# Optimization experiments

Measured on AMD Instinct MI355X. Metric: run time of the kernel, lower is better.

## Reference

```python
import jax, jax.numpy as jnp
import numpy as np

DECAY_EPS = 1e-8  # matches F.cosine_similarity eps
DECAY_RATE = 0.999  # buffer decay_rate


def setup_inputs() -> dict:
    key = jax.random.key(0)
    ks = jax.random.split(key, 6)
    B, M, D = 256, 65536, 1024
    return {
        "query": jax.random.normal(ks[0], (B, D), dtype=jnp.float32),
        "mem_keys": jax.random.normal(ks[1], (M, D), dtype=jnp.float32),
        "mem_values": jax.random.normal(ks[2], (M, D), dtype=jnp.float32),
        "importance": jax.random.uniform(ks[3], (M,), dtype=jnp.float32),
        "access_times": jax.random.randint(ks[4], (M,), 0, 1000, dtype=jnp.int32),
        "access_counts": jax.random.randint(ks[5], (M,), 1, 50, dtype=jnp.int32),
        "current_time": 1000,
        "top_k": 8,
    }


def reference(query, mem_keys, mem_values, importance, access_times, access_counts, current_time, top_k):
    # Batched version of AdaptiveMemoryBuffer.retrieve.
    # query: [B, D]; mem_keys/mem_values: [M, D]; importance/access_*: [M]
    qn = query / jnp.maximum(jnp.linalg.norm(query, axis=-1, keepdims=True), DECAY_EPS)
    kn = mem_keys / jnp.maximum(jnp.linalg.norm(mem_keys, axis=-1, keepdims=True), DECAY_EPS)
    sim = qn @ kn.T  # [B, M] cosine similarity

    dt = (current_time - access_times).astype(jnp.float32)           # time since access
    retention = jnp.power(jnp.float32(DECAY_RATE), dt)               # forgetting curve
    freq_bonus = jnp.log1p(access_counts.astype(jnp.float32))        # log(1 + count)
    scores = sim * (retention * importance * freq_bonus)[None, :]    # [B, M]

    top_scores, top_idx = jax.lax.top_k(scores, top_k)                # [B, k]
    weights = jax.nn.softmax(top_scores, axis=-1)                     # [B, k]
    combined = jnp.einsum('bk,bkd->bd', weights, mem_values[top_idx]) # weighted gather
    confidence = weights.max(axis=-1)                                 # [B]
    return combined, confidence
```

## Files before the change

kernel.cpp:

```cpp
#include <hip/hip_runtime.h>
#include <hip/hip_bf16.h>
#include <math.h>
#include <float.h>

typedef __attribute__((ext_vector_type(8))) short short8;
typedef __attribute__((ext_vector_type(4))) float f32x4;

namespace {

constexpr int B = 256;
constexpr int M = 65536;
constexpr int D = 1024;
constexpr float DECAY_EPS = 1e-8f;
constexpr float DECAY_RATE = 0.999f;

constexpr int BN = 64;
constexpr int BK = 32;
constexpr int KSTEPS = D / BK;

constexpr int CHUNKS = 8;
constexpr int CHUNK = M / CHUNKS;
constexpr int NCAND = CHUNKS * 8;

__device__ inline ushort f2bf(float f) {
  union { __hip_bfloat16 h; ushort u; } v;
  v.h = __float2bfloat16(f);
  return v.u;
}

__global__ void prep_q_kernel(const float* __restrict__ q, ushort* __restrict__ qnf) {
  const int r = blockIdx.x;
  const int t = threadIdx.x;
  float4 v = reinterpret_cast<const float4*>(q + (size_t)r * D)[t];
  float ss = v.x * v.x + v.y * v.y + v.z * v.z + v.w * v.w;
#pragma unroll
  for (int off = 32; off; off >>= 1) ss += __shfl_down(ss, off, 64);
  __shared__ float red[4];
  if ((t & 63) == 0) red[t >> 6] = ss;
  __syncthreads();
  const float inv = 1.0f / fmaxf(sqrtf(red[0] + red[1] + red[2] + red[3]), DECAY_EPS);
  ushort4 o;
  o.x = f2bf(v.x * inv); o.y = f2bf(v.y * inv);
  o.z = f2bf(v.z * inv); o.w = f2bf(v.w * inv);
  const int k0 = t * 4;
  const int kt = k0 >> 5;
  const int lane_slot = (r & 15) + 16 * ((k0 & 31) >> 3);
  const int j0 = k0 & 7;
  *reinterpret_cast<ushort4*>(qnf + (size_t)(kt * 16 + (r >> 4)) * 512 + lane_slot * 8 + j0) = o;
}

__global__ __launch_bounds__(256) void score_gemm_kernel(
    const ushort* __restrict__ qnf, const float* __restrict__ keys,
    const float* __restrict__ importance, const int* __restrict__ atimes,
    const int* __restrict__ acnts, const int* __restrict__ ctime,
    float* __restrict__ scores) {
  __shared__ alignas(16) ushort Bs[2][BN * BK];
  __shared__ float cscale[BN];

  const int t = threadIdx.x;
  const int lane = t & 63;
  const int w = t >> 6;
  const int jb = blockIdx.x * BN;

  const int rw = t >> 2;
  const int cw = t & 3;
  const float* kptr = keys + (size_t)(jb + rw) * D + cw * 8;
  const int woff = rw * BK + ((cw ^ ((rw >> 1) & 3)) * 8);

  f32x4 acc[4][4];
#pragma unroll
  for (int f = 0; f < 4; ++f)
#pragma unroll
    for (int n = 0; n < 4; ++n) acc[f][n] = (f32x4)(0.0f);

  float kn2 = 0.0f;

  {
    float4 v0 = *reinterpret_cast<const float4*>(kptr);
    float4 v1 = *reinterpret_cast<const float4*>(kptr + 4);
    kn2 += v0.x * v0.x + v0.y * v0.y + v0.z * v0.z + v0.w * v0.w;
    kn2 += v1.x * v1.x + v1.y * v1.y + v1.z * v1.z + v1.w * v1.w;
    short8 pk;
    pk[0] = (short)f2bf(v0.x); pk[1] = (short)f2bf(v0.y);
    pk[2] = (short)f2bf(v0.z); pk[3] = (short)f2bf(v0.w);
    pk[4] = (short)f2bf(v1.x); pk[5] = (short)f2bf(v1.y);
    pk[6] = (short)f2bf(v1.z); pk[7] = (short)f2bf(v1.w);
    *reinterpret_cast<short8*>(&Bs[0][woff]) = pk;
  }
  __syncthreads();

  int roff[4];
#pragma unroll
  for (int nf = 0; nf < 4; ++nf) {
    const int row = nf * 16 + (lane & 15);
    roff[nf] = row * BK + (((lane >> 4) ^ ((row >> 1) & 3)) * 8);
  }

  for (int kt = 0; kt < KSTEPS; ++kt) {
    const int cur = kt & 1;
    float4 nv0, nv1;
    if (kt + 1 < KSTEPS) {
      nv0 = *reinterpret_cast<const float4*>(kptr + (kt + 1) * BK);
      nv1 = *reinterpret_cast<const float4*>(kptr + (kt + 1) * BK + 4);
    }
    short8 a[4];
    const short8* ap = reinterpret_cast<const short8*>(qnf) + (size_t)(kt * 16 + w * 4) * 64 + lane;
#pragma unroll
    for (int f = 0; f < 4; ++f) a[f] = ap[f * 64];
    short8 bb[4];
#pragma unroll
    for (int nf = 0; nf < 4; ++nf)
      bb[nf] = *reinterpret_cast<const short8*>(&Bs[cur][roff[nf]]);
#pragma unroll
    for (int f = 0; f < 4; ++f)
#pragma unroll
      for (int nf = 0; nf < 4; ++nf)
        acc[f][nf] = __builtin_amdgcn_mfma_f32_16x16x32_bf16(a[f], bb[nf], acc[f][nf], 0, 0, 0);
    if (kt + 1 < KSTEPS) {
      kn2 += nv0.x * nv0.x + nv0.y * nv0.y + nv0.z * nv0.z + nv0.w * nv0.w;
      kn2 += nv1.x * nv1.x + nv1.y * nv1.y + nv1.z * nv1.z + nv1.w * nv1.w;
      short8 pk;
      pk[0] = (short)f2bf(nv0.x); pk[1] = (short)f2bf(nv0.y);
      pk[2] = (short)f2bf(nv0.z); pk[3] = (short)f2bf(nv0.w);
      pk[4] = (short)f2bf(nv1.x); pk[5] = (short)f2bf(nv1.y);
      pk[6] = (short)f2bf(nv1.z); pk[7] = (short)f2bf(nv1.w);
      *reinterpret_cast<short8*>(&Bs[cur ^ 1][woff]) = pk;
    }
    __syncthreads();
  }

  kn2 += __shfl_xor(kn2, 1, 64);
  kn2 += __shfl_xor(kn2, 2, 64);
  if (cw == 0) {
    const int j = jb + rw;
    const float dt = (float)(ctime[0] - atimes[j]);
    const float mult = powf(DECAY_RATE, dt) * importance[j] * log1pf((float)acnts[j]);
    cscale[rw] = mult / fmaxf(sqrtf(kn2), DECAY_EPS);
  }
  __syncthreads();

#pragma unroll
  for (int f = 0; f < 4; ++f) {
    const int row0 = (w * 4 + f) * 16 + ((lane >> 4) << 2);
#pragma unroll
    for (int nf = 0; nf < 4; ++nf) {
      const int col = nf * 16 + (lane & 15);
      const float cs = cscale[col];
#pragma unroll
      for (int rr = 0; rr < 4; ++rr)
        scores[(size_t)(row0 + rr) * M + jb + col] = acc[f][nf][rr] * cs;
    }
  }
}

__global__ __launch_bounds__(256) void topk_partial_kernel(
    const float* __restrict__ scores, int* __restrict__ cand_i) {
  const int b = blockIdx.y;
  const int c = blockIdx.x;
  const int t = threadIdx.x;
  const int lane = t & 63, w = t >> 6;
  const float4* base4 = reinterpret_cast<const float4*>(scores + (size_t)b * M + (size_t)c * CHUNK);

  float s8[8];
  int i8[8];
#pragma unroll
  for (int i = 0; i < 8; ++i) { s8[i] = -FLT_MAX; i8[i] = 0; }

  auto ins = [&](float x, int j) {
    if (x > s8[0]) {
#pragma unroll
      for (int i = 0; i < 8; ++i) {
        const bool up = (i < 7) && (x > s8[i + 1]);
        const float ks = (x > s8[i]) ? x : s8[i];
        const int ki = (x > s8[i]) ? j : i8[i];
        s8[i] = up ? s8[i + 1] : ks;
        i8[i] = up ? i8[i + 1] : ki;
      }
    }
  };

  const int jbase = c * CHUNK;
  for (int it = 0; it < CHUNK / (256 * 4); ++it) {
    const int slot = it * 256 + t;
    const float4 v = base4[slot];
    const int j0 = jbase + slot * 4;
    ins(v.x, j0 + 0);
    ins(v.y, j0 + 1);
    ins(v.z, j0 + 2);
    ins(v.w, j0 + 3);
  }

  __shared__ float ls[2048];
  __shared__ int li[2048];
#pragma unroll
  for (int i = 0; i < 8; ++i) { ls[t * 8 + i] = s8[i]; li[t * 8 + i] = i8[i]; }
  __syncthreads();

  __shared__ float rs4[4];
  __shared__ int rp4[4];
  for (int r = 0; r < 8; ++r) {
    float ms = -FLT_MAX;
    int mp = 0;
#pragma unroll
    for (int i = 0; i < 8; ++i) {
      const float v = ls[i * 256 + t];
      if (v > ms) { ms = v; mp = i * 256 + t; }
    }
#pragma unroll
    for (int off = 32; off; off >>= 1) {
      const float ov = __shfl_xor(ms, off, 64);
      const int op = __shfl_xor(mp, off, 64);
      if (ov > ms) { ms = ov; mp = op; }
    }
    if (lane == 0) { rs4[w] = ms; rp4[w] = mp; }
    __syncthreads();
    if (t == 0) {
      float bs = -FLT_MAX;
      int bp = 0;
#pragma unroll
      for (int i = 0; i < 4; ++i)
        if (rs4[i] > bs) { bs = rs4[i]; bp = rp4[i]; }
      cand_i[((size_t)b * CHUNKS + c) * 8 + r] = li[bp];
      ls[bp] = -FLT_MAX;
    }
    __syncthreads();
  }
}

__global__ __launch_bounds__(512) void rescore_kernel(
    const int* __restrict__ cand_i, const float* __restrict__ query,
    const float* __restrict__ keys, const float* __restrict__ values,
    const float* __restrict__ importance, const int* __restrict__ atimes,
    const int* __restrict__ acnts, const int* __restrict__ ctime,
    float* __restrict__ outc, float* __restrict__ conf) {
  const int b = blockIdx.x;
  const int t = threadIdx.x;
  const int lane = t & 63, w = t >> 6;

  const float4* qv4 = reinterpret_cast<const float4*>(query + (size_t)b * D + lane * 16);
  float4 q0 = qv4[0], q1 = qv4[1], q2 = qv4[2], q3 = qv4[3];
  float ssq = q0.x * q0.x + q0.y * q0.y + q0.z * q0.z + q0.w * q0.w
            + q1.x * q1.x + q1.y * q1.y + q1.z * q1.z + q1.w * q1.w
            + q2.x * q2.x + q2.y * q2.y + q2.z * q2.z + q2.w * q2.w
            + q3.x * q3.x + q3.y * q3.y + q3.z * q3.z + q3.w * q3.w;
#pragma unroll
  for (int off = 32; off; off >>= 1) ssq += __shfl_xor(ssq, off, 64);
  const float qdn = fmaxf(sqrtf(ssq), DECAY_EPS);
  const int ct = ctime[0];

  __shared__ float sc[NCAND];
  __shared__ int sidx[NCAND];

  for (int u = 0; u < 8; ++u) {
    const int c = w * 8 + u;
    const int j = cand_i[(size_t)b * NCAND + c];
    const float4* kv4 = reinterpret_cast<const float4*>(keys + (size_t)j * D + lane * 16);
    const float4 k0 = kv4[0], k1 = kv4[1], k2 = kv4[2], k3 = kv4[3];
    float dd = q0.x * k0.x + q0.y * k0.y + q0.z * k0.z + q0.w * k0.w
             + q1.x * k1.x + q1.y * k1.y + q1.z * k1.z + q1.w * k1.w
             + q2.x * k2.x + q2.y * k2.y + q2.z * k2.z + q2.w * k2.w
             + q3.x * k3.x + q3.y * k3.y + q3.z * k3.z + q3.w * k3.w;
    float nn = k0.x * k0.x + k0.y * k0.y + k0.z * k0.z + k0.w * k0.w
             + k1.x * k1.x + k1.y * k1.y + k1.z * k1.z + k1.w * k1.w
             + k2.x * k2.x + k2.y * k2.y + k2.z * k2.z + k2.w * k2.w
             + k3.x * k3.x + k3.y * k3.y + k3.z * k3.z + k3.w * k3.w;
#pragma unroll
    for (int off = 32; off; off >>= 1) {
      dd += __shfl_xor(dd, off, 64);
      nn += __shfl_xor(nn, off, 64);
    }
    if (lane == 0) {
      const float dtv = (float)(ct - atimes[j]);
      const float mult = powf(DECAY_RATE, dtv) * importance[j] * log1pf((float)acnts[j]);
      sc[c] = dd / (qdn * fmaxf(sqrtf(nn), DECAY_EPS)) * mult;
      sidx[c] = j;
    }
  }
  __syncthreads();

  __shared__ float w8s[8];
  __shared__ int g8[8];
  __shared__ float confv;
  __shared__ float tls[8];
  __shared__ int tli[8];
  if (w == 0) {
    float myv = sc[lane];
    for (int r = 0; r < 8; ++r) {
      float m = myv;
      int mi = lane;
#pragma unroll
      for (int off = 32; off; off >>= 1) {
        const float ov = __shfl_xor(m, off, 64);
        const int oi = __shfl_xor(mi, off, 64);
        if (ov > m || (ov == m && oi < mi)) { m = ov; mi = oi; }
      }
      if (lane == 0) { tls[r] = m; tli[r] = mi; }
      if (lane == mi) myv = -FLT_MAX;
    }
    if (lane == 0) {
      const float mx = tls[0];
      float e[8];
      float z = 0.0f;
#pragma unroll
      for (int r = 0; r < 8; ++r) { e[r] = expf(tls[r] - mx); z += e[r]; }
      const float invz = 1.0f / z;
#pragma unroll
      for (int r = 0; r < 8; ++r) { w8s[r] = e[r] * invz; g8[r] = sidx[tli[r]]; }
      confv = w8s[0];
    }
  }
  __syncthreads();

  float2 acc = make_float2(0.0f, 0.0f);
#pragma unroll
  for (int k = 0; k < 8; ++k) {
    const float wk = w8s[k];
    const float2 v = *reinterpret_cast<const float2*>(values + (size_t)g8[k] * D + 2 * t);
    acc.x = fmaf(wk, v.x, acc.x);
    acc.y = fmaf(wk, v.y, acc.y);
  }
  *reinterpret_cast<float2*>(outc + (size_t)b * D + 2 * t) = acc;
  if (t == 0) conf[b] = confv;
}

}

extern "C" void kernel_launch(void* const* d_in, const int* in_sizes, int n_in,
                              void* d_out, int out_size, void* d_ws, size_t ws_size,
                              hipStream_t stream) {
  const float* query = (const float*)d_in[0];
  const float* keys = (const float*)d_in[1];
  const float* values = (const float*)d_in[2];
  const float* importance = (const float*)d_in[3];
  const int* atimes = (const int*)d_in[4];
  const int* acnts = (const int*)d_in[5];
  const int* ctime = (const int*)d_in[6];

  float* out = (float*)d_out;
  ushort* qnf = (ushort*)d_ws;
  float* scores = (float*)((char*)d_ws + (size_t)B * D * sizeof(ushort));
  int* cand = (int*)(scores + (size_t)B * M);

  prep_q_kernel<<<B, 256, 0, stream>>>(query, qnf);
  score_gemm_kernel<<<M / BN, 256, 0, stream>>>(qnf, keys, importance, atimes,
                                                acnts, ctime, scores);
  dim3 gA(CHUNKS, B);
  topk_partial_kernel<<<gA, 256, 0, stream>>>(scores, cand);
  rescore_kernel<<<B, 512, 0, stream>>>(cand, query, keys, values, importance,
                                        atimes, acnts, ctime, out, out + (size_t)B * D);
}
```

Baseline: 171.3 us.

## Double K-tile depth and prefetch keys two stages ahead in score GEMM

Raises the GEMM K-tile from 32 to 64, halving the number of barrier-separated iterations. Restructures the loop so the fp32 key tile is loaded two stages ahead and the A fragments one stage ahead, with a new XOR swizzle for the wider LDS rows. It also replaces the HIP bf16 conversion with a manual round-to-nearest-even bit trick. The aim is to hide global-memory latency and cut sync overhead, at the cost of more registers, which could lower occupancy.

```diff
diff --git a/kernel.cpp b/kernel.cpp
--- a/kernel.cpp
+++ b/kernel.cpp
@@ -1,5 +1,4 @@
 #include <hip/hip_runtime.h>
-#include <hip/hip_bf16.h>
 #include <math.h>
 #include <float.h>
 
@@ -15,7 +14,7 @@
 constexpr float DECAY_RATE = 0.999f;
 
 constexpr int BN = 64;
-constexpr int BK = 32;
+constexpr int BK = 64;
 constexpr int KSTEPS = D / BK;
 
 constexpr int CHUNKS = 8;
@@ -23,9 +22,9 @@
 constexpr int NCAND = CHUNKS * 8;
 
 __device__ inline ushort f2bf(float f) {
-  union { __hip_bfloat16 h; ushort u; } v;
-  v.h = __float2bfloat16(f);
-  return v.u;
+  union { float f; unsigned u; } v; v.f = f;
+  unsigned r = v.u + 0x7fffu + ((v.u >> 16) & 1u);
+  return (ushort)(r >> 16);
 }
 
 __global__ void prep_q_kernel(const float* __restrict__ q, ushort* __restrict__ qnf) {
@@ -64,8 +63,20 @@
 
   const int rw = t >> 2;
   const int cw = t & 3;
-  const float* kptr = keys + (size_t)(jb + rw) * D + cw * 8;
-  const int woff = rw * BK + ((cw ^ ((rw >> 1) & 3)) * 8);
+  const float4* kp4 = reinterpret_cast<const float4*>(keys + (size_t)(jb + rw) * D) + cw * 4;
+
+  const int wo0 = rw * BK + (((2 * cw) ^ (rw & 7)) * 8);
+  const int wo1 = rw * BK + (((2 * cw + 1) ^ (rw & 7)) * 8);
+
+  int roff[2][4];
+#pragma unroll
+  for (int ks = 0; ks < 2; ++ks)
+#pragma unroll
+    for (int nf = 0; nf < 4; ++nf) {
+      const int row = nf * 16 + (lane & 15);
+      const int slot = ks * 4 + (lane >> 4);
+      roff[ks][nf] = row * BK + ((slot ^ (row & 7)) * 8);
+    }
 
   f32x4 acc[4][4];
 #pragma unroll
@@ -74,57 +85,63 @@
     for (int n = 0; n < 4; ++n) acc[f][n] = (f32x4)(0.0f);
 
   float kn2 = 0.0f;
-
-  {
-    float4 v0 = *reinterpret_cast<const float4*>(kptr);
-    float4 v1 = *reinterpret_cast<const float4*>(kptr + 4);
-    kn2 += v0.x * v0.x + v0.y * v0.y + v0.z * v0.z + v0.w * v0.w;
-    kn2 += v1.x * v1.x + v1.y * v1.y + v1.z * v1.z + v1.w * v1.w;
-    short8 pk;
-    pk[0] = (short)f2bf(v0.x); pk[1] = (short)f2bf(v0.y);
-    pk[2] = (short)f2bf(v0.z); pk[3] = (short)f2bf(v0.w);
-    pk[4] = (short)f2bf(v1.x); pk[5] = (short)f2bf(v1.y);
-    pk[6] = (short)f2bf(v1.z); pk[7] = (short)f2bf(v1.w);
-    *reinterpret_cast<short8*>(&Bs[0][woff]) = pk;
-  }
-  __syncthreads();
-
-  int roff[4];
-#pragma unroll
-  for (int nf = 0; nf < 4; ++nf) {
-    const int row = nf * 16 + (lane & 15);
-    roff[nf] = row * BK + (((lane >> 4) ^ ((row >> 1) & 3)) * 8);
-  }
-
-  for (int kt = 0; kt < KSTEPS; ++kt) {
-    const int cur = kt & 1;
-    float4 nv0, nv1;
-    if (kt + 1 < KSTEPS) {
-      nv0 = *reinterpret_cast<const float4*>(kptr + (kt + 1) * BK);
-      nv1 = *reinterpret_cast<const float4*>(kptr + (kt + 1) * BK + 4);
-    }
-    short8 a[4];
-    const short8* ap = reinterpret_cast<const short8*>(qnf) + (size_t)(kt * 16 + w * 4) * 64 + lane;
-#pragma unroll
-    for (int f = 0; f < 4; ++f) a[f] = ap[f * 64];
-    short8 bb[4];
-#pragma unroll
-    for (int nf = 0; nf < 4; ++nf)
-      bb[nf] = *reinterpret_cast<const short8*>(&Bs[cur][roff[nf]]);
-#pragma unroll
-    for (int f = 0; f < 4; ++f)
+  short8 a[2][4];
+  float4 bv[4];
+
+  const short8* apbase = reinterpret_cast<const short8*>(qnf);
+
+  auto loadA = [&](int s) {
+#pragma unroll
+    for (int ks = 0; ks < 2; ++ks)
+#pragma unroll
+      for (int f = 0; f < 4; ++f)
+        a[ks][f] = apbase[(size_t)((2 * s + ks) * 16 + w * 4 + f) * 64 + lane];
+  };
+  auto loadB = [&](int s) {
+#pragma unroll
+    for (int i = 0; i < 4; ++i) bv[i] = kp4[s * 16 + i];
+  };
+  auto stageB = [&](int buf) {
+#pragma unroll
+    for (int i = 0; i < 4; ++i)
+      kn2 += bv[i].x * bv[i].x + bv[i].y * bv[i].y + bv[i].z * bv[i].z + bv[i].w * bv[i].w;
+    short8 p0, p1;
+    p0[0] = (short)f2bf(bv[0].x); p0[1] = (short)f2bf(bv[0].y);
+    p0[2] = (short)f2bf(bv[0].z); p0[3] = (short)f2bf(bv[0].w);
+    p0[4] = (short)f2bf(bv[1].x); p0[5] = (short)f2bf(bv[1].y);
+    p0[6] = (short)f2bf(bv[1].z); p0[7] = (short)f2bf(bv[1].w);
+    p1[0] = (short)f2bf(bv[2].x); p1[1] = (short)f2bf(bv[2].y);
+    p1[2] = (short)f2bf(bv[2].z); p1[3] = (short)f2bf(bv[2].w);
+    p1[4] = (short)f2bf(bv[3].x); p1[5] = (short)f2bf(bv[3].y);
+    p1[6] = (short)f2bf(bv[3].z); p1[7] = (short)f2bf(bv[3].w);
+    *reinterpret_cast<short8*>(&Bs[buf][wo0]) = p0;
+    *reinterpret_cast<short8*>(&Bs[buf][wo1]) = p1;
+  };
+
+  loadB(0);
+  stageB(0);
+  loadA(0);
+  loadB(1);
+  __syncthreads();
+
+  for (int s = 0; s < KSTEPS; ++s) {
+    const int cur = s & 1;
+#pragma unroll
+    for (int ks = 0; ks < 2; ++ks) {
+      short8 bf[4];
 #pragma unroll
       for (int nf = 0; nf < 4; ++nf)
-        acc[f][nf] = __builtin_amdgcn_mfma_f32_16x16x32_bf16(a[f], bb[nf], acc[f][nf], 0, 0, 0);
-    if (kt + 1 < KSTEPS) {
-      kn2 += nv0.x * nv0.x + nv0.y * nv0.y + nv0.z * nv0.z + nv0.w * nv0.w;
-      kn2 += nv1.x * nv1.x + nv1.y * nv1.y + nv1.z * nv1.z + nv1.w * nv1.w;
-      short8 pk;
-      pk[0] = (short)f2bf(nv0.x); pk[1] = (short)f2bf(nv0.y);
-      pk[2] = (short)f2bf(nv0.z); pk[3] = (short)f2bf(nv0.w);
-      pk[4] = (short)f2bf(nv1.x); pk[5] = (short)f2bf(nv1.y);
-      pk[6] = (short)f2bf(nv1.z); pk[7] = (short)f2bf(nv1.w);
-      *reinterpret_cast<short8*>(&Bs[cur ^ 1][woff]) = pk;
+        bf[nf] = *reinterpret_cast<const short8*>(&Bs[cur][roff[ks][nf]]);
+#pragma unroll
+      for (int f = 0; f < 4; ++f)
+#pragma unroll
+        for (int nf = 0; nf < 4; ++nf)
+          acc[f][nf] = __builtin_amdgcn_mfma_f32_16x16x32_bf16(a[ks][f], bf[nf], acc[f][nf], 0, 0, 0);
+    }
+    if (s + 1 < KSTEPS) {
+      loadA(s + 1);
+      stageB(cur ^ 1);
+      if (s + 2 < KSTEPS) loadB(s + 2);
     }
     __syncthreads();
   }
```

New measurement: 150.3 us. 1.14x faster.

## Store scores as bf16 and pack the top-k key with its index

Applied to the files above, without the earlier changes.

The score GEMM now writes the intermediate score matrix as bf16 instead of fp32, which halves the traffic written by the GEMM and read back by the top-k pass. The top-k pass packs an order-preserving 16-bit score key together with a 16-bit index into one uint, so it no longer keeps separate index arrays. The GEMM tile is also changed from 64 to 32 key rows per block with 512 threads, and fp32-to-bf16 rounding is done by hand with bit tricks. The risk is that bf16 scores coarsen the candidate ranking: near-ties may select different candidates before the exact rescore.

```diff
diff --git a/kernel.cpp b/kernel.cpp
--- a/kernel.cpp
+++ b/kernel.cpp
@@ -1,9 +1,9 @@
 #include <hip/hip_runtime.h>
-#include <hip/hip_bf16.h>
 #include <math.h>
 #include <float.h>
 
 typedef __attribute__((ext_vector_type(8))) short short8;
+typedef __attribute__((ext_vector_type(8))) ushort ushort8;
 typedef __attribute__((ext_vector_type(4))) float f32x4;
 
 namespace {
@@ -14,7 +14,7 @@
 constexpr float DECAY_EPS = 1e-8f;
 constexpr float DECAY_RATE = 0.999f;
 
-constexpr int BN = 64;
+constexpr int BN = 32;
 constexpr int BK = 32;
 constexpr int KSTEPS = D / BK;
 
@@ -23,9 +23,9 @@
 constexpr int NCAND = CHUNKS * 8;
 
 __device__ inline ushort f2bf(float f) {
-  union { __hip_bfloat16 h; ushort u; } v;
-  v.h = __float2bfloat16(f);
-  return v.u;
+  union { float f; unsigned u; } v; v.f = f;
+  unsigned r = v.u + 0x7fffu + ((v.u >> 16) & 1u);
+  return (ushort)(r >> 16);
 }
 
 __global__ void prep_q_kernel(const float* __restrict__ q, ushort* __restrict__ qnf) {
@@ -49,89 +49,74 @@
   *reinterpret_cast<ushort4*>(qnf + (size_t)(kt * 16 + (r >> 4)) * 512 + lane_slot * 8 + j0) = o;
 }
 
-__global__ __launch_bounds__(256) void score_gemm_kernel(
+__global__ __launch_bounds__(512, 8) void score_gemm_kernel(
     const ushort* __restrict__ qnf, const float* __restrict__ keys,
     const float* __restrict__ importance, const int* __restrict__ atimes,
     const int* __restrict__ acnts, const int* __restrict__ ctime,
-    float* __restrict__ scores) {
+    ushort* __restrict__ scores) {
   __shared__ alignas(16) ushort Bs[2][BN * BK];
   __shared__ float cscale[BN];
 
   const int t = threadIdx.x;
   const int lane = t & 63;
   const int w = t >> 6;
+  const int h = lane >> 4;
+  const int q = lane & 15;
   const int jb = blockIdx.x * BN;
 
-  const int rw = t >> 2;
-  const int cw = t & 3;
-  const float* kptr = keys + (size_t)(jb + rw) * D + cw * 8;
-  const int woff = rw * BK + ((cw ^ ((rw >> 1) & 3)) * 8);
-
-  f32x4 acc[4][4];
-#pragma unroll
-  for (int f = 0; f < 4; ++f)
-#pragma unroll
-    for (int n = 0; n < 4; ++n) acc[f][n] = (f32x4)(0.0f);
+  const int rw = t >> 4;
+  const int cw = t & 15;
+  const float2* kp2 = reinterpret_cast<const float2*>(keys + (size_t)(jb + rw) * D) + cw;
+  const int wo = rw * BK + (((cw >> 2) ^ ((rw >> 1) & 3)) * 4 + (cw & 3)) * 2;
+
+  int roff[2];
+#pragma unroll
+  for (int nf = 0; nf < 2; ++nf) {
+    const int row = nf * 16 + q;
+    roff[nf] = row * BK + ((h ^ ((row >> 1) & 3)) * 8);
+  }
+
+  f32x4 acc[2][2];
+#pragma unroll
+  for (int f = 0; f < 2; ++f)
+#pragma unroll
+    for (int n = 0; n < 2; ++n) acc[f][n] = (f32x4)(0.0f);
 
   float kn2 = 0.0f;
-
-  {
-    float4 v0 = *reinterpret_cast<const float4*>(kptr);
-    float4 v1 = *reinterpret_cast<const float4*>(kptr + 4);
-    kn2 += v0.x * v0.x + v0.y * v0.y + v0.z * v0.z + v0.w * v0.w;
-    kn2 += v1.x * v1.x + v1.y * v1.y + v1.z * v1.z + v1.w * v1.w;
-    short8 pk;
-    pk[0] = (short)f2bf(v0.x); pk[1] = (short)f2bf(v0.y);
-    pk[2] = (short)f2bf(v0.z); pk[3] = (short)f2bf(v0.w);
-    pk[4] = (short)f2bf(v1.x); pk[5] = (short)f2bf(v1.y);
-    pk[6] = (short)f2bf(v1.z); pk[7] = (short)f2bf(v1.w);
-    *reinterpret_cast<short8*>(&Bs[0][woff]) = pk;
-  }
-  __syncthreads();
-
-  int roff[4];
-#pragma unroll
-  for (int nf = 0; nf < 4; ++nf) {
-    const int row = nf * 16 + (lane & 15);
-    roff[nf] = row * BK + (((lane >> 4) ^ ((row >> 1) & 3)) * 8);
-  }
-
-  for (int kt = 0; kt < KSTEPS; ++kt) {
-    const int cur = kt & 1;
-    float4 nv0, nv1;
-    if (kt + 1 < KSTEPS) {
-      nv0 = *reinterpret_cast<const float4*>(kptr + (kt + 1) * BK);
-      nv1 = *reinterpret_cast<const float4*>(kptr + (kt + 1) * BK + 4);
-    }
-    short8 a[4];
-    const short8* ap = reinterpret_cast<const short8*>(qnf) + (size_t)(kt * 16 + w * 4) * 64 + lane;
-#pragma unroll
-    for (int f = 0; f < 4; ++f) a[f] = ap[f * 64];
-    short8 bb[4];
-#pragma unroll
-    for (int nf = 0; nf < 4; ++nf)
-      bb[nf] = *reinterpret_cast<const short8*>(&Bs[cur][roff[nf]]);
-#pragma unroll
-    for (int f = 0; f < 4; ++f)
-#pragma unroll
-      for (int nf = 0; nf < 4; ++nf)
-        acc[f][nf] = __builtin_amdgcn_mfma_f32_16x16x32_bf16(a[f], bb[nf], acc[f][nf], 0, 0, 0);
-    if (kt + 1 < KSTEPS) {
-      kn2 += nv0.x * nv0.x + nv0.y * nv0.y + nv0.z * nv0.z + nv0.w * nv0.w;
-      kn2 += nv1.x * nv1.x + nv1.y * nv1.y + nv1.z * nv1.z + nv1.w * nv1.w;
-      short8 pk;
-      pk[0] = (short)f2bf(nv0.x); pk[1] = (short)f2bf(nv0.y);
-      pk[2] = (short)f2bf(nv0.z); pk[3] = (short)f2bf(nv0.w);
-      pk[4] = (short)f2bf(nv1.x); pk[5] = (short)f2bf(nv1.y);
-      pk[6] = (short)f2bf(nv1.z); pk[7] = (short)f2bf(nv1.w);
-      *reinterpret_cast<short8*>(&Bs[cur ^ 1][woff]) = pk;
+  float2 nv;
+
+  nv = kp2[0];
+  kn2 += nv.x * nv.x + nv.y * nv.y;
+  *reinterpret_cast<uint*>(&Bs[0][wo]) = (uint)f2bf(nv.x) | ((uint)f2bf(nv.y) << 16);
+  nv = kp2[16];
+  __syncthreads();
+
+  const short8* apbase = reinterpret_cast<const short8*>(qnf);
+
+  for (int s = 0; s < KSTEPS; ++s) {
+    const int cur = s & 1;
+    short8 a0 = apbase[(size_t)(s * 16 + 2 * w + 0) * 64 + lane];
+    short8 a1 = apbase[(size_t)(s * 16 + 2 * w + 1) * 64 + lane];
+    short8 b0 = *reinterpret_cast<const short8*>(&Bs[cur][roff[0]]);
+    short8 b1 = *reinterpret_cast<const short8*>(&Bs[cur][roff[1]]);
+    acc[0][0] = __builtin_amdgcn_mfma_f32_16x16x32_bf16(a0, b0, acc[0][0], 0, 0, 0);
+    acc[0][1] = __builtin_amdgcn_mfma_f32_16x16x32_bf16(a0, b1, acc[0][1], 0, 0, 0);
+    acc[1][0] = __builtin_amdgcn_mfma_f32_16x16x32_bf16(a1, b0, acc[1][0], 0, 0, 0);
+    acc[1][1] = __builtin_amdgcn_mfma_f32_16x16x32_bf16(a1, b1, acc[1][1], 0, 0, 0);
+    if (s + 1 < KSTEPS) {
+      kn2 += nv.x * nv.x + nv.y * nv.y;
+      *reinterpret_cast<uint*>(&Bs[cur ^ 1][wo]) =
+          (uint)f2bf(nv.x) | ((uint)f2bf(nv.y) << 16);
+      if (s + 2 < KSTEPS) nv = kp2[(s + 2) * 16];
     }
     __syncthreads();
   }
 
   kn2 += __shfl_xor(kn2, 1, 64);
   kn2 += __shfl_xor(kn2, 2, 64);
-  if (cw == 0) {
+  kn2 += __shfl_xor(kn2, 4, 64);
+  kn2 += __shfl_xor(kn2, 8, 64);
+  if (q == 0) {
     const int j = jb + rw;
     const float dt = (float)(ctime[0] - atimes[j]);
     const float mult = powf(DECAY_RATE, dt) * importance[j] * log1pf((float)acnts[j]);
@@ -140,88 +125,94 @@
   __syncthreads();
 
 #pragma unroll
-  for (int f = 0; f < 4; ++f) {
-    const int row0 = (w * 4 + f) * 16 + ((lane >> 4) << 2);
-#pragma unroll
-    for (int nf = 0; nf < 4; ++nf) {
-      const int col = nf * 16 + (lane & 15);
-      const float cs = cscale[col];
-#pragma unroll
-      for (int rr = 0; rr < 4; ++rr)
-        scores[(size_t)(row0 + rr) * M + jb + col] = acc[f][nf][rr] * cs;
+  for (int f = 0; f < 2; ++f) {
+    const int row0 = (2 * w + f) * 16 + (h << 2);
+#pragma unroll
+    for (int nf = 0; nf < 2; ++nf) {
+      const float cs = cscale[nf * 16 + q];
+#pragma unroll
+      for (int rr = 0; rr < 4; ++rr) {
+        const float v = acc[f][nf][rr] * cs;
+        const float vn = __shfl_xor(v, 1, 64);
+        if (!(q & 1)) {
+          const uint pk = (uint)f2bf(v) | ((uint)f2bf(vn) << 16);
+          *reinterpret_cast<uint*>(
+              scores + (size_t)(row0 + rr) * M + jb + nf * 16 + q) = pk;
+        }
+      }
     }
   }
 }
 
 __global__ __launch_bounds__(256) void topk_partial_kernel(
-    const float* __restrict__ scores, int* __restrict__ cand_i) {
+    const ushort* __restrict__ scores, int* __restrict__ cand_i) {
   const int b = blockIdx.y;
   const int c = blockIdx.x;
   const int t = threadIdx.x;
   const int lane = t & 63, w = t >> 6;
-  const float4* base4 = reinterpret_cast<const float4*>(scores + (size_t)b * M + (size_t)c * CHUNK);
-
-  float s8[8];
-  int i8[8];
-#pragma unroll
-  for (int i = 0; i < 8; ++i) { s8[i] = -FLT_MAX; i8[i] = 0; }
-
-  auto ins = [&](float x, int j) {
+  const ushort8* base8 =
+      reinterpret_cast<const ushort8*>(scores + (size_t)b * M + (size_t)c * CHUNK);
+
+  uint s8[8];
+#pragma unroll
+  for (int i = 0; i < 8; ++i) s8[i] = 0;
+
+  auto ins = [&](uint x) {
     if (x > s8[0]) {
 #pragma unroll
       for (int i = 0; i < 8; ++i) {
         const bool up = (i < 7) && (x > s8[i + 1]);
-        const float ks = (x > s8[i]) ? x : s8[i];
-        const int ki = (x > s8[i]) ? j : i8[i];
-        s8[i] = up ? s8[i + 1] : ks;
-        i8[i] = up ? i8[i + 1] : ki;
+        const uint keep = (x > s8[i]) ? x : s8[i];
+        s8[i] = up ? s8[i + 1] : keep;
       }
     }
   };
 
-  const int jbase = c * CHUNK;
-  for (int it = 0; it < CHUNK / (256 * 4); ++it) {
+  const uint jbase = (uint)c * CHUNK;
+#pragma unroll
+  for (int it = 0; it < CHUNK / (256 * 8); ++it) {
     const int slot = it * 256 + t;
-    const float4 v = base4[slot];
-    const int j0 = jbase + slot * 4;
-    ins(v.x, j0 + 0);
-    ins(v.y, j0 + 1);
-    ins(v.z, j0 + 2);
-    ins(v.w, j0 + 3);
-  }
-
-  __shared__ float ls[2048];
-  __shared__ int li[2048];
-#pragma unroll
-  for (int i = 0; i < 8; ++i) { ls[t * 8 + i] = s8[i]; li[t * 8 + i] = i8[i]; }
-  __syncthreads();
-
-  __shared__ float rs4[4];
+    const ushort8 v = base8[slot];
+    const uint j0 = jbase + (uint)slot * 8;
+#pragma unroll
+    for (int e = 0; e < 8; ++e) {
+      const ushort s = (ushort)v[e];
+      const ushort key = (s & 0x8000) ? (ushort)~s : (ushort)(s | 0x8000);
+      ins(((uint)key << 16) | ((j0 + e) & 0xFFFFu));
+    }
+  }
+
+  __shared__ uint ls[2048];
+#pragma unroll
+  for (int i = 0; i < 8; ++i) ls[t * 8 + i] = s8[i];
+  __syncthreads();
+
+  __shared__ uint rs4[4];
   __shared__ int rp4[4];
   for (int r = 0; r < 8; ++r) {
-    float ms = -FLT_MAX;
+    uint ms = 0;
     int mp = 0;
 #pragma unroll
     for (int i = 0; i < 8; ++i) {
-      const float v = ls[i * 256 + t];
+      const uint v = ls[i * 256 + t];
       if (v > ms) { ms = v; mp = i * 256 + t; }
     }
 #pragma unroll
     for (int off = 32; off; off >>= 1) {
-      const float ov = __shfl_xor(ms, off, 64);
+      const uint ov = __shfl_xor(ms, off, 64);
       const int op = __shfl_xor(mp, off, 64);
       if (ov > ms) { ms = ov; mp = op; }
     }
     if (lane == 0) { rs4[w] = ms; rp4[w] = mp; }
     __syncthreads();
     if (t == 0) {
-      float bs = -FLT_MAX;
+      uint bs = 0;
       int bp = 0;
 #pragma unroll
       for (int i = 0; i < 4; ++i)
         if (rs4[i] > bs) { bs = rs4[i]; bp = rp4[i]; }
-      cand_i[((size_t)b * CHUNKS + c) * 8 + r] = li[bp];
-      ls[bp] = -FLT_MAX;
+      cand_i[((size_t)b * CHUNKS + c) * 8 + r] = (int)(ls[bp] & 0xFFFFu);
+      ls[bp] = 0;
     }
     __syncthreads();
   }
@@ -338,11 +329,11 @@
 
   float* out = (float*)d_out;
   ushort* qnf = (ushort*)d_ws;
-  float* scores = (float*)((char*)d_ws + (size_t)B * D * sizeof(ushort));
+  ushort* scores = qnf + (size_t)B * D;
   int* cand = (int*)(scores + (size_t)B * M);
 
   prep_q_kernel<<<B, 256, 0, stream>>>(query, qnf);
-  score_gemm_kernel<<<M / BN, 256, 0, stream>>>(qnf, keys, importance, atimes,
+  score_gemm_kernel<<<M / BN, 512, 0, stream>>>(qnf, keys, importance, atimes,
                                                 acnts, ctime, scores);
   dim3 gA(CHUNKS, B);
   topk_partial_kernel<<<gA, 256, 0, stream>>>(scores, cand);
```

Measured after the change: 163.6 us. 4.5% less time.
